# Performance work log

Measured on AMD Instinct MI355X. Metric: run time of the kernel, lower is better.

Reference implementation:

```python
import jax, jax.numpy as jnp
import numpy as np

B, T, N = 32, 64, 2048
HID, HEADS, DH, BOT, MAX_LAG = 256, 8, 32, 64, 7


def setup_inputs() -> dict:
    key = jax.random.key(0)
    ks = jax.random.split(key, 12)
    def nrm(k, shape, s=0.05):
        return jax.random.normal(k, shape, jnp.float32) * s
    # delay logits init as in the module: log(softmaxed exp decay)
    w = np.exp(-np.arange(MAX_LAG + 1) / 3.0)
    w = w / w.sum()
    delay_logits = jnp.asarray(np.log(w + 1e-8), jnp.float32)
    # row-normalized adjacency prior (done in __init__ of the module)
    adj_raw = jax.random.uniform(ks[0], (N, N), jnp.float32)
    adj_prior = adj_raw / (adj_raw.sum(-1, keepdims=True) + 1e-8)
    return {
        "x": jax.random.normal(ks[1], (B, T, N), jnp.float32),
        "features": jax.random.normal(ks[2], (B, N, HID), jnp.float32),
        "delay_logits": delay_logits,
        "w_dp": nrm(ks[3], (1, HID)), "b_dp": jnp.zeros((HID,), jnp.float32),
        "w_qkv_low": nrm(ks[4], (HID, 3 * BOT)), "b_qkv_low": jnp.zeros((3 * BOT,), jnp.float32),
        "w_qkv_high": nrm(ks[5], (3 * BOT, 3 * HID)), "b_qkv_high": jnp.zeros((3 * HID,), jnp.float32),
        "w_out_low": nrm(ks[6], (HID, BOT)), "b_out_low": jnp.zeros((BOT,), jnp.float32),
        "w_out_high": nrm(ks[7], (BOT, HID)), "b_out_high": jnp.zeros((HID,), jnp.float32),
        "adj_prior": adj_prior,
        "geo_weight": jnp.array([0.3], jnp.float32),
        "ln_gamma": jnp.ones((HID,), jnp.float32),
        "ln_beta": jnp.zeros((HID,), jnp.float32),
    }


def reference(x, features, delay_logits, w_dp, b_dp,
              w_qkv_low, b_qkv_low, w_qkv_high, b_qkv_high,
              w_out_low, b_out_low, w_out_high, b_out_high,
              adj_prior, geo_weight, ln_gamma, ln_beta):
    # --- delay-weighted signal (generation interval) ---
    dw = jax.nn.softmax(delay_logits)                      # [max_lag+1]
    taus = min(MAX_LAG + 1, T)                              # static
    x_lags = jnp.flip(x, axis=1)[:, :taus]                  # [B,taus,N], lag tau = x[:, -(tau+1)]
    delayed = jnp.einsum('t,btn->bn', dw[:taus], x_lags)    # [B,N]
    delay_feat = delayed[:, :, None] * w_dp[0] + b_dp       # Linear(1, hidden)
    combined = features + 0.1 * delay_feat                  # [B,N,HID]

    # --- low-rank QKV ---
    qkv = (combined @ w_qkv_low + b_qkv_low) @ w_qkv_high + b_qkv_high  # [B,N,3*HID]
    q, k, v = jnp.split(qkv, 3, axis=-1)
    def to_heads(t):
        return t.reshape(B, N, HEADS, DH).transpose(0, 2, 1, 3)  # [B,H,N,dh]
    q, k, v = to_heads(q), to_heads(k), to_heads(v)

    # --- linear attention (elu+1 feature map, O(N)) ---
    qf = jax.nn.elu(q) + 1.0
    kf = jax.nn.elu(k) + 1.0
    kv = jnp.einsum('bhnd,bhne->bhde', kf, v)               # [B,H,dh,dh]
    k_sum = kf.sum(axis=2) + 1e-8                           # [B,H,dh]
    num = jnp.einsum('bhnd,bhde->bhne', qf, kv)             # [B,H,N,dh]
    den = jnp.einsum('bhnd,bhd->bhn', qf, k_sum)[..., None] + 1e-8
    attended = num / den

    # --- geo-adjacency blend ---
    gb = jax.nn.sigmoid(geo_weight[0])
    v_geo = jnp.einsum('nm,bhmd->bhnd', adj_prior, v)       # dense graph mixing
    attended = (1.0 - gb) * attended + gb * v_geo

    attended = attended.transpose(0, 2, 1, 3).reshape(B, N, HID)
    # dropout is identity in eval mode
    out = (attended @ w_out_low + b_out_low) @ w_out_high + b_out_high

    # --- residual + LayerNorm ---
    y = out + features
    mu = y.mean(-1, keepdims=True)
    var = ((y - mu) ** 2).mean(-1, keepdims=True)
    return (y - mu) / jnp.sqrt(var + 1e-5) * ln_gamma + ln_beta
```

## Files before the change

kernel.cpp:

```cpp
#include <hip/hip_runtime.h>
#include <hip/hip_bf16.h>
#include <stdint.h>

typedef unsigned short u16;
typedef float f4v __attribute__((ext_vector_type(4)));
typedef short s8v __attribute__((ext_vector_type(8)));


__device__ __forceinline__ float bf2f(u16 u) {
  union { float f; uint32_t i; } x; x.i = ((uint32_t)u) << 16; return x.f;
}
__device__ __forceinline__ u16 f2bf(float f) {
  uint32_t u = __float_as_uint(f);
  u = (u + 0x7FFFu + ((u >> 16) & 1u)) >> 16;
  return (u16)u;
}
__device__ __forceinline__ uint32_t pk2(float a, float b) {
  return (uint32_t)f2bf(a) | ((uint32_t)f2bf(b) << 16);
}
__device__ __forceinline__ void gload16(const void* g, void* l) {
  __builtin_amdgcn_global_load_lds((const __attribute__((address_space(1))) void*)g,
                                   (__attribute__((address_space(3))) void*)l, 16, 0, 0);
}

__global__ __launch_bounds__(256) void prep_all_k(
    const float* __restrict__ x, const float* __restrict__ dlog,
    const float* __restrict__ w_dp, const float* __restrict__ b_dp,
    const float* __restrict__ wql, const float* __restrict__ bql,
    const float* __restrict__ wqh, const float* __restrict__ wol,
    const float* __restrict__ bqh,
    float* __restrict__ wl_d, float* __restrict__ bl_p, float* __restrict__ delayed,
    u16* __restrict__ wqlT, u16* __restrict__ wqhT, u16* __restrict__ wvlT,
    float* __restrict__ cvl) {
  const int bid = blockIdx.x, t = threadIdx.x;
  if (bid < 256) {
    float mx = dlog[0];
#pragma unroll
    for (int i = 1; i < 8; ++i) mx = fmaxf(mx, dlog[i]);
    float w8[8], ssum = 0.f;
#pragma unroll
    for (int i = 0; i < 8; ++i) { w8[i] = __expf(dlog[i] - mx); ssum += w8[i]; }
    float inv = 1.f / ssum;
    int r = bid * 256 + t;
    int b = r >> 11, n = r & 2047;
    const float* xb = x + (size_t)b * 64 * 2048;
    float acc = 0.f;
#pragma unroll
    for (int tau = 0; tau < 8; ++tau) acc += w8[tau] * inv * xb[(size_t)(63 - tau) * 2048 + n];
    delayed[r] = acc;
  } else if (bid < 512) {
    int n = bid - 256;
    wqlT[(size_t)n * 256 + t] = f2bf(n < 192 ? wql[(size_t)t * 192 + n] : 0.f);
  } else if (bid < 1280) {
    int n = bid - 512;
    if (t < 192) wqhT[(size_t)n * 192 + t] = f2bf(wqh[(size_t)t * 768 + n]);
  } else if (bid < 1408) {
    int d = bid - 1280;
    __shared__ float wolc[256];
    if (d < 64) wolc[t] = wol[(size_t)t * 64 + d];
    __syncthreads();
    if (t < 192) {
      float s = 0.f;
      if (d < 64) {
        const float* wr = wqh + (size_t)t * 768 + 512;
        for (int c = 0; c < 256; ++c) s = fmaf(wr[c], wolc[c], s);
      }
      wvlT[(size_t)d * 192 + t] = f2bf(s);
    }
    if (t == 0 && d < 64) {
      float s = 0.f;
      for (int c = 0; c < 256; ++c) s = fmaf(bqh[512 + c], wolc[c], s);
      cvl[d] = s;
    }
  } else {
    if (t < 192) {
      float s1 = 0.f, s2 = 0.f;
      for (int k = 0; k < 256; ++k) {
        float w = wql[k * 192 + t];
        s1 += w_dp[k] * w;
        s2 += b_dp[k] * w;
      }
      wl_d[t] = 0.1f * s1;
      bl_p[t] = bql[t] + 0.1f * s2;
    }
  }
}

struct MArgs {
  const u16* A;
  const float* Af32;
  const u16* Bt;
  const float* delayed; const float* wl_d; const float* bl_p;
  const float* bqh;
  const float* cvl;
  u16* low; u16* qf; u16* kf; u16* v; u16* vpt;
  u16* geopart;
};

enum { GLOW = 0, GQ = 1, GKV = 2, GGEO = 3, GVP = 4 };

template <int MODE>
__global__ __launch_bounds__(256) void mgemm_k(MArgs ma) {
  constexpr int KLOOP = (MODE == GLOW) ? 256 : (MODE == GGEO) ? 512 : 192;
  constexpr int LDA = (MODE == GLOW) ? 256 : (MODE == GGEO) ? 2048 : 192;
  constexpr int LDB = (MODE == GLOW) ? 256 : (MODE == GGEO) ? 2048 : 192;
  constexpr bool SWAPPED = (MODE == GLOW || MODE == GQ || MODE == GGEO);

  constexpr int SHN = (MODE == GKV) ? (128 * 136) : (128 * 128);
  __shared__ __align__(16) u16 SH[SHN];
  u16* Al = SH;
  u16* Bl = SH + 128 * 64;

  const int t = threadIdx.x;
  const int l = t & 63, w = t >> 6;
  const int wm = w >> 1, wn = w & 1;

  int ct, rt, bz = 0;
  if constexpr (MODE == GGEO) {
    int lin = blockIdx.x + 16 * blockIdx.y + 256 * blockIdx.z;
    int xcd = lin & 7, idx = lin >> 3;
    ct = idx & 15;
    int pid = xcd * 8 + (idx >> 4);
    rt = pid & 15;
    bz = pid >> 4;
  } else {
    constexpr int NCT = (MODE == GLOW || MODE == GQ) ? 2 : (MODE == GKV) ? 4 : 1;
    int lin = blockIdx.x + NCT * blockIdx.y;
    int xcd = lin & 7, idx = lin >> 3;
    ct = idx % NCT; rt = xcd * 64 + idx / NCT;
  }
  const int kbase = (MODE == GGEO) ? bz * 512 : 0;

  f4v acc[4][4] = {};

  for (int k0 = 0; k0 < KLOOP; k0 += 64) {
    __syncthreads();
#pragma unroll
    for (int s = 0; s < 4; ++s) {
      int c = s * 256 + t;
      int r = c >> 3, cc = c & 7;
      int g = ((cc & 3) ^ ((r >> 1) & 3)) | ((cc & 4) ^ ((r & 1) << 2));
      int row = rt * 128 + r;
      int kg = kbase + k0 + g * 8;
      if constexpr (MODE == GLOW || MODE == GGEO) {
        const float* src = ma.Af32 + (size_t)row * LDA + kg;
        float4 x0 = *(const float4*)src;
        float4 x1 = *(const float4*)(src + 4);
        uint4 qq = {pk2(x0.x, x0.y), pk2(x0.z, x0.w), pk2(x1.x, x1.y), pk2(x1.z, x1.w)};
        *(uint4*)&Al[c * 8] = qq;
      } else {
        gload16(ma.A + (size_t)row * LDA + kg, (char*)Al + (s * 4 + w) * 1024);
      }
      gload16(ma.Bt + (size_t)(ct * 128 + r) * LDB + kg,
              (char*)Bl + (s * 4 + w) * 1024);
    }
    __syncthreads();

#pragma unroll
    for (int kk = 0; kk < 64; kk += 32) {
      s8v fa[4], fb[4];
#pragma unroll
      for (int mr = 0; mr < 4; ++mr) {
        int ra = wm * 64 + mr * 16 + (l & 15);
        int ch = ((l >> 4) ^ ((ra >> 1) & 3)) | ((kk >> 3) ^ ((ra & 1) << 2));
        fa[mr] = *(const s8v*)(Al + ra * 64 + ch * 8);
      }
#pragma unroll
      for (int nr = 0; nr < 4; ++nr) {
        int rb = wn * 64 + nr * 16 + (l & 15);
        int cb = ((l >> 4) ^ ((rb >> 1) & 3)) | ((kk >> 3) ^ ((rb & 1) << 2));
        fb[nr] = *(const s8v*)(Bl + rb * 64 + cb * 8);
      }
      if constexpr (SWAPPED) {
#pragma unroll
        for (int mr = 0; mr < 4; ++mr)
#pragma unroll
          for (int nr = 0; nr < 4; ++nr)
            acc[mr][nr] = __builtin_amdgcn_mfma_f32_16x16x32_bf16(fb[nr], fa[mr], acc[mr][nr], 0, 0, 0);
      } else {
#pragma unroll
        for (int mr = 0; mr < 4; ++mr)
#pragma unroll
          for (int nr = 0; nr < 4; ++nr)
            acc[mr][nr] = __builtin_amdgcn_mfma_f32_16x16x32_bf16(fa[mr], fb[nr], acc[mr][nr], 0, 0, 0);
      }
    }
  }

  const int r0 = rt * 128 + wm * 64, c0 = ct * 128 + wn * 64;

  if constexpr (MODE == GVP) {
    const int lr = (l >> 4) * 4, lc = l & 15;
#pragma unroll
    for (int mr = 0; mr < 4; ++mr)
#pragma unroll
      for (int nr = 0; nr < 4; ++nr) {
        if (wn == 0) {
          int d = nr * 16 + lc;
          float cadd = ma.cvl[d];
          int n0 = (r0 + mr * 16 + lr) & 2047;
          int b = rt >> 4;
          ushort4 st = {f2bf(acc[mr][nr][0] + cadd), f2bf(acc[mr][nr][1] + cadd),
                        f2bf(acc[mr][nr][2] + cadd), f2bf(acc[mr][nr][3] + cadd)};
          *(ushort4*)(ma.vpt + ((size_t)(b * 64 + d)) * 2048 + n0) = st;
        }
      }
  } else if constexpr (MODE == GKV) {
    const int lr = (l >> 4) * 4, lc = l & 15;
    const bool isK = (ct < 2);
    __syncthreads();
#pragma unroll
    for (int nr = 0; nr < 4; ++nr) {
      int chat_l = wn * 64 + nr * 16 + lc;
      float bias = ma.bqh[256 + ct * 128 + chat_l];
#pragma unroll
      for (int mr = 0; mr < 4; ++mr) {
        int n_l = wm * 64 + mr * 16 + lr;
        float v0 = acc[mr][nr][0] + bias;
        float v1 = acc[mr][nr][1] + bias;
        float v2 = acc[mr][nr][2] + bias;
        float v3 = acc[mr][nr][3] + bias;
        if (isK) {
          v0 = (v0 > 0.f) ? (v0 + 1.f) : __expf(v0);
          v1 = (v1 > 0.f) ? (v1 + 1.f) : __expf(v1);
          v2 = (v2 > 0.f) ? (v2 + 1.f) : __expf(v2);
          v3 = (v3 > 0.f) ? (v3 + 1.f) : __expf(v3);
        }
        ushort4 st = {f2bf(v0), f2bf(v1), f2bf(v2), f2bf(v3)};
        *(ushort4*)&SH[chat_l * 136 + n_l] = st;
      }
    }
    __syncthreads();
    const int b = rt >> 4, nbase = (rt & 15) * 128;
#pragma unroll
    for (int s = 0; s < 8; ++s) {
      int idx = s * 256 + t;
      int chat_l = idx >> 4, nch = (idx & 15) * 8;
      uint4 q = *(const uint4*)&SH[chat_l * 136 + nch];
      int chat_g = ct * 128 + chat_l;
      u16* dst = isK ? (ma.kf + ((size_t)(b * 256 + chat_g)) * 2048)
                     : (ma.v + ((size_t)(b * 256 + chat_g - 256)) * 2048);
      *(uint4*)(dst + nbase + nch) = q;
    }
  } else {
    const int rowl = l & 15, colq = (l >> 4) * 4;
#pragma unroll
    for (int mr = 0; mr < 4; ++mr) {
      int row = r0 + mr * 16 + rowl;
#pragma unroll
      for (int nr = 0; nr < 4; ++nr) {
        int col0 = c0 + nr * 16 + colq;
        if constexpr (MODE == GLOW) {
          if (col0 < 192) {
            float dl = ma.delayed[row];
            float4 wd = *(const float4*)(ma.wl_d + col0);
            float4 bp = *(const float4*)(ma.bl_p + col0);
            ushort4 st = {f2bf(acc[mr][nr][0] + dl * wd.x + bp.x),
                          f2bf(acc[mr][nr][1] + dl * wd.y + bp.y),
                          f2bf(acc[mr][nr][2] + dl * wd.z + bp.z),
                          f2bf(acc[mr][nr][3] + dl * wd.w + bp.w)};
            *(ushort4*)(ma.low + (size_t)row * 192 + col0) = st;
          }
        } else if constexpr (MODE == GQ) {
          float4 bias = *(const float4*)(ma.bqh + col0);
          float v0 = acc[mr][nr][0] + bias.x;
          float v1 = acc[mr][nr][1] + bias.y;
          float v2 = acc[mr][nr][2] + bias.z;
          float v3 = acc[mr][nr][3] + bias.w;
          v0 = (v0 > 0.f) ? (v0 + 1.f) : __expf(v0);
          v1 = (v1 > 0.f) ? (v1 + 1.f) : __expf(v1);
          v2 = (v2 > 0.f) ? (v2 + 1.f) : __expf(v2);
          v3 = (v3 > 0.f) ? (v3 + 1.f) : __expf(v3);
          ushort4 st = {f2bf(v0), f2bf(v1), f2bf(v2), f2bf(v3)};
          *(ushort4*)(ma.qf + (size_t)row * 256 + col0) = st;
        } else {
          u16* dst = ma.geopart + (size_t)bz * 4194304;
          ushort4 st = {f2bf(acc[mr][nr][0]), f2bf(acc[mr][nr][1]),
                        f2bf(acc[mr][nr][2]), f2bf(acc[mr][nr][3])};
          *(ushort4*)(dst + (size_t)row * 2048 + col0) = st;
        }
      }
    }
  }
}

__global__ __launch_bounds__(256) void kvred_k(const u16* __restrict__ kfT,
                                               const u16* __restrict__ vT,
                                               float* __restrict__ kvpart,
                                               float* __restrict__ kspart) {
  const int z = blockIdx.x, h = blockIdx.y, b = blockIdx.z;
  const int t = threadIdx.x, l = t & 63, w = t >> 6;
  const size_t base = ((size_t)(b * 256 + h * 32)) * 2048 + z * 512 + w * 128;
  const u16* ka = kfT + base;
  const u16* vb = vT + base;
  f4v acc[2][2] = {};
  float ks[2] = {0.f, 0.f};
#pragma unroll
  for (int s = 0; s < 4; ++s) {
    int koff = s * 32 + (l >> 4) * 8;
    s8v fa[2], fb[2];
#pragma unroll
    for (int mr = 0; mr < 2; ++mr)
      fa[mr] = *(const s8v*)(ka + (size_t)(mr * 16 + (l & 15)) * 2048 + koff);
#pragma unroll
    for (int nr = 0; nr < 2; ++nr)
      fb[nr] = *(const s8v*)(vb + (size_t)(nr * 16 + (l & 15)) * 2048 + koff);
#pragma unroll
    for (int mr = 0; mr < 2; ++mr) {
      float sacc = 0.f;
#pragma unroll
      for (int j = 0; j < 8; ++j) sacc += bf2f((u16)fa[mr][j]);
      ks[mr] += sacc;
    }
#pragma unroll
    for (int mr = 0; mr < 2; ++mr)
#pragma unroll
      for (int nr = 0; nr < 2; ++nr)
        acc[mr][nr] = __builtin_amdgcn_mfma_f32_16x16x32_bf16(fa[mr], fb[nr], acc[mr][nr], 0, 0, 0);
  }
  ks[0] += __shfl_xor(ks[0], 16); ks[0] += __shfl_xor(ks[0], 32);
  ks[1] += __shfl_xor(ks[1], 16); ks[1] += __shfl_xor(ks[1], 32);

  __shared__ float kvs[4][32][32];
  __shared__ float kss[4][32];
#pragma unroll
  for (int mr = 0; mr < 2; ++mr)
#pragma unroll
    for (int nr = 0; nr < 2; ++nr)
#pragma unroll
      for (int i = 0; i < 4; ++i)
        kvs[w][mr * 16 + (l >> 4) * 4 + i][nr * 16 + (l & 15)] = acc[mr][nr][i];
  if (l < 16) { kss[w][l] = ks[0]; kss[w][16 + l] = ks[1]; }
  __syncthreads();
  float* kvp = kvpart + ((size_t)(z * 256 + b * 8 + h)) * 1024;
#pragma unroll
  for (int q = 0; q < 4; ++q) {
    int idx = q * 256 + t;
    kvp[idx] = kvs[0][idx >> 5][idx & 31] + kvs[1][idx >> 5][idx & 31] +
               kvs[2][idx >> 5][idx & 31] + kvs[3][idx >> 5][idx & 31];
  }
  if (t < 32)
    kspart[((size_t)(z * 256 + b * 8 + h)) * 32 + t] =
        kss[0][t] + kss[1][t] + kss[2][t] + kss[3][t];
}

__global__ __launch_bounds__(256) void gfin_k(const u16* __restrict__ qf,
                                              const float* __restrict__ rden,
                                              const u16* __restrict__ geopart,
                                              const u16* __restrict__ B2t,
                                              const float* __restrict__ cvec,
                                              const float* __restrict__ feats,
                                              const float* __restrict__ gamma,
                                              const float* __restrict__ beta,
                                              float* __restrict__ y) {
  __shared__ __align__(16) u16 Al[64 * 64];
  __shared__ __align__(16) u16 Bl[256 * 64];
  __shared__ float LN1[4][64], LN2[4][64];

  const int t = threadIdx.x;
  const int l = t & 63, w = t >> 6;
  const int rt = blockIdx.x;
  const int b = rt >> 5;

  f4v acc[4][4] = {};

  for (int k0 = 0; k0 < 320; k0 += 64) {
    __syncthreads();
#pragma unroll
    for (int s = 0; s < 2; ++s) {
      int c = s * 256 + t;
      int r = c >> 3, cc = c & 7;
      int g = ((cc & 3) ^ ((r >> 1) & 3)) | ((cc & 4) ^ ((r & 1) << 2));
      int row = rt * 64 + r;
      int kg = k0 + g * 8;
      if (k0 < 256) {
        float sc = rden[(size_t)row * 8 + (kg >> 5)];
        s8v qv = *(const s8v*)(qf + (size_t)row * 256 + kg);
        uint4 qq = {pk2(bf2f((u16)qv[0]) * sc, bf2f((u16)qv[1]) * sc),
                    pk2(bf2f((u16)qv[2]) * sc, bf2f((u16)qv[3]) * sc),
                    pk2(bf2f((u16)qv[4]) * sc, bf2f((u16)qv[5]) * sc),
                    pk2(bf2f((u16)qv[6]) * sc, bf2f((u16)qv[7]) * sc)};
        *(uint4*)&Al[c * 8] = qq;
      } else {
        int n = row & 2047;
        const u16* gp = geopart + (size_t)n * 2048 + b * 64 + (kg - 256);
        s8v p0 = *(const s8v*)(gp);
        s8v p1 = *(const s8v*)(gp + 4194304);
        s8v p2 = *(const s8v*)(gp + 8388608);
        s8v p3 = *(const s8v*)(gp + 12582912);
        float vv[8];
#pragma unroll
        for (int j = 0; j < 8; ++j)
          vv[j] = bf2f((u16)p0[j]) + bf2f((u16)p1[j]) + bf2f((u16)p2[j]) + bf2f((u16)p3[j]);
        uint4 qq = {pk2(vv[0], vv[1]), pk2(vv[2], vv[3]), pk2(vv[4], vv[5]), pk2(vv[6], vv[7])};
        *(uint4*)&Al[c * 8] = qq;
      }
    }
#pragma unroll
    for (int s = 0; s < 8; ++s) {
      int c = s * 256 + t;
      int r = c >> 3, cc = c & 7;
      int g = ((cc & 3) ^ ((r >> 1) & 3)) | ((cc & 4) ^ ((r & 1) << 2));
      gload16(B2t + ((size_t)b * 256 + r) * 320 + k0 + g * 8,
              (char*)Bl + (s * 4 + w) * 1024);
    }
    __syncthreads();

#pragma unroll
    for (int kk = 0; kk < 64; kk += 32) {
      s8v fa[4], fb[4];
#pragma unroll
      for (int mr = 0; mr < 4; ++mr) {
        int ra = mr * 16 + (l & 15);
        int ch = ((l >> 4) ^ ((ra >> 1) & 3)) | ((kk >> 3) ^ ((ra & 1) << 2));
        fa[mr] = *(const s8v*)(Al + ra * 64 + ch * 8);
      }
#pragma unroll
      for (int nr = 0; nr < 4; ++nr) {
        int rb = w * 64 + nr * 16 + (l & 15);
        int cb = ((l >> 4) ^ ((rb >> 1) & 3)) | ((kk >> 3) ^ ((rb & 1) << 2));
        fb[nr] = *(const s8v*)(Bl + rb * 64 + cb * 8);
      }
#pragma unroll
      for (int mr = 0; mr < 4; ++mr)
#pragma unroll
        for (int nr = 0; nr < 4; ++nr)
          acc[mr][nr] = __builtin_amdgcn_mfma_f32_16x16x32_bf16(fb[nr], fa[mr], acc[mr][nr], 0, 0, 0);
    }
  }

  const int rowl = l & 15, colq = (l >> 4) * 4;
  float s1v[4] = {0.f, 0.f, 0.f, 0.f}, s2v[4] = {0.f, 0.f, 0.f, 0.f};
#pragma unroll
  for (int mr = 0; mr < 4; ++mr) {
    int row = rt * 64 + mr * 16 + rowl;
#pragma unroll
    for (int nr = 0; nr < 4; ++nr) {
      int col0 = w * 64 + nr * 16 + colq;
      float4 cv = *(const float4*)(cvec + col0);
      float4 ft = *(const float4*)(feats + (size_t)row * 256 + col0);
      f4v vv = acc[mr][nr];
      vv[0] += cv.x + ft.x; vv[1] += cv.y + ft.y;
      vv[2] += cv.z + ft.z; vv[3] += cv.w + ft.w;
      acc[mr][nr] = vv;
      s1v[mr] += vv[0] + vv[1] + vv[2] + vv[3];
      s2v[mr] += vv[0] * vv[0] + vv[1] * vv[1] + vv[2] * vv[2] + vv[3] * vv[3];
    }
  }
#pragma unroll
  for (int mr = 0; mr < 4; ++mr) {
    s1v[mr] += __shfl_xor(s1v[mr], 16); s2v[mr] += __shfl_xor(s2v[mr], 16);
    s1v[mr] += __shfl_xor(s1v[mr], 32); s2v[mr] += __shfl_xor(s2v[mr], 32);
  }
  if (l < 16) {
#pragma unroll
    for (int mr = 0; mr < 4; ++mr) {
      LN1[w][mr * 16 + l] = s1v[mr];
      LN2[w][mr * 16 + l] = s2v[mr];
    }
  }
  __syncthreads();
#pragma unroll
  for (int mr = 0; mr < 4; ++mr) {
    int rl = mr * 16 + rowl;
    int row = rt * 64 + rl;
    float s1 = LN1[0][rl] + LN1[1][rl] + LN1[2][rl] + LN1[3][rl];
    float s2 = LN2[0][rl] + LN2[1][rl] + LN2[2][rl] + LN2[3][rl];
    float mu = s1 * (1.f / 256.f);
    float var = s2 * (1.f / 256.f) - mu * mu;
    float rstd = rsqrtf(fmaxf(var, 0.f) + 1e-5f);
#pragma unroll
    for (int nr = 0; nr < 4; ++nr) {
      int col0 = w * 64 + nr * 16 + colq;
      float4 g4 = *(const float4*)(gamma + col0);
      float4 b4 = *(const float4*)(beta + col0);
      f4v vv = acc[mr][nr];
      float4 o;
      o.x = (vv[0] - mu) * rstd * g4.x + b4.x;
      o.y = (vv[1] - mu) * rstd * g4.y + b4.y;
      o.z = (vv[2] - mu) * rstd * g4.z + b4.z;
      o.w = (vv[3] - mu) * rstd * g4.w + b4.w;
      *(float4*)(y + (size_t)row * 256 + col0) = o;
    }
  }
}

__global__ __launch_bounds__(64) void mmat_k(const float* __restrict__ kvpart,
                                             const float* __restrict__ wol,
                                             const float* __restrict__ geow,
                                             float* __restrict__ Mm) {
  const int bh = blockIdx.x;
  const int h = bh & 7, b = bh >> 3;
  const int c = threadIdx.x;
  __shared__ float kvs[32][32];
  for (int i = c; i < 1024; i += 64) {
    float s = 0.f;
#pragma unroll
    for (int p = 0; p < 4; ++p) s += kvpart[(size_t)(p * 256 + bh) * 1024 + i];
    kvs[i >> 5][i & 31] = s;
  }
  __syncthreads();
  float one_m = 1.f - 1.f / (1.f + __expf(-geow[0]));
  float acc[32];
#pragma unroll
  for (int d = 0; d < 32; ++d) acc[d] = 0.f;
  for (int e = 0; e < 32; ++e) {
    float w = wol[(size_t)(h * 32 + e) * 64 + c];
#pragma unroll
    for (int d = 0; d < 32; ++d) acc[d] = fmaf(kvs[d][e], w, acc[d]);
  }
  float* mp = Mm + (size_t)b * 16384 + (size_t)h * 32 * 64 + c;
#pragma unroll
  for (int d = 0; d < 32; ++d) mp[d * 64] = one_m * acc[d];
}

__global__ __launch_bounds__(256) void bprep_k(const float* __restrict__ Mm,
                                               const float* __restrict__ woh,
                                               const float* __restrict__ bol,
                                               const float* __restrict__ boh,
                                               const float* __restrict__ geow,
                                               u16* __restrict__ B2t,
                                               float* __restrict__ cvec) {
  const int kt = blockIdx.x, b = blockIdx.y;
  const int c = threadIdx.x;
  __shared__ float Ms[64][64];
#pragma unroll
  for (int i = 0; i < 16; ++i) {
    int flat = c + i * 256;
    int kk = flat >> 6, e = flat & 63;
    Ms[kk][e] = Mm[(size_t)b * 16384 + (size_t)(kt * 64 + kk) * 64 + e];
  }
  __syncthreads();
  float wcol[64];
#pragma unroll
  for (int e = 0; e < 64; ++e) wcol[e] = woh[(size_t)e * 256 + c];
  u16* dst = B2t + ((size_t)b * 256 + c) * 320;
  for (int kk = 0; kk < 64; ++kk) {
    float s = 0.f;
#pragma unroll
    for (int e = 0; e < 64; ++e) s = fmaf(Ms[kk][e], wcol[e], s);
    dst[kt * 64 + kk] = f2bf(s);
  }
  if (kt == 0) {
    float gb = 1.f / (1.f + __expf(-geow[0]));
#pragma unroll
    for (int d = 0; d < 64; ++d) dst[256 + d] = f2bf(gb * wcol[d]);
    if (b == 0) {
      float s = boh[c];
#pragma unroll
      for (int d = 0; d < 64; ++d) s = fmaf(bol[d], wcol[d], s);
      cvec[c] = s;
    }
  }
}

__global__ __launch_bounds__(256) void rden_k(const u16* __restrict__ qf,
                                              const float* __restrict__ kspart,
                                              float* __restrict__ rden) {
  const int t = threadIdx.x;
  const int b = (blockIdx.x * 16) >> 11;
  __shared__ float ksumf[256];
  {
    int h = t >> 5, e = t & 31;
    float s = 0.f;
#pragma unroll
    for (int p = 0; p < 4; ++p) s += kspart[(size_t)(p * 256 + b * 8 + h) * 32 + e];
    ksumf[t] = s + 1e-8f;
  }
  __syncthreads();
  const int row = blockIdx.x * 16 + (t >> 4);
  const int c0 = (t & 15) * 16;
  s8v q0 = *(const s8v*)(qf + (size_t)row * 256 + c0);
  s8v q1 = *(const s8v*)(qf + (size_t)row * 256 + c0 + 8);
  float part = 0.f;
#pragma unroll
  for (int j = 0; j < 8; ++j) part = fmaf(bf2f((u16)q0[j]), ksumf[c0 + j], part);
#pragma unroll
  for (int j = 0; j < 8; ++j) part = fmaf(bf2f((u16)q1[j]), ksumf[c0 + 8 + j], part);
  float den = part + __shfl_xor(part, 1);
  if ((t & 1) == 0) rden[(size_t)row * 8 + (c0 >> 5)] = 1.f / (den + 1e-8f);
}

extern "C" void kernel_launch(void* const* d_in, const int* in_sizes, int n_in,
                              void* d_out, int out_size, void* d_ws, size_t ws_size,
                              hipStream_t stream) {
  const float* x     = (const float*)d_in[0];
  const float* feats = (const float*)d_in[1];
  const float* dlog  = (const float*)d_in[2];
  const float* w_dp  = (const float*)d_in[3];
  const float* b_dp  = (const float*)d_in[4];
  const float* wql   = (const float*)d_in[5];
  const float* bql   = (const float*)d_in[6];
  const float* wqh   = (const float*)d_in[7];
  const float* bqh   = (const float*)d_in[8];
  const float* wol   = (const float*)d_in[9];
  const float* bol   = (const float*)d_in[10];
  const float* woh   = (const float*)d_in[11];
  const float* boh   = (const float*)d_in[12];
  const float* adj   = (const float*)d_in[13];
  const float* geow  = (const float*)d_in[14];
  const float* gamma = (const float*)d_in[15];
  const float* beta  = (const float*)d_in[16];

  char* ws = (char*)d_ws;
  constexpr size_t OFF_WLD   = 1024;
  constexpr size_t OFF_BLP   = 2048;
  constexpr size_t OFF_CVEC  = 4096;
  constexpr size_t OFF_CVL   = 5120;
  constexpr size_t OFF_DEL   = 8192;
  constexpr size_t OFF_WQLT  = 270336;
  constexpr size_t OFF_WQHT  = 401408;
  constexpr size_t OFF_WVLT  = 696320;
  constexpr size_t OFF_KSP   = 745472;
  constexpr size_t OFF_RDEN  = 876544;
  constexpr size_t OFF_MM    = 2973696;
  constexpr size_t OFF_B2T   = 5070848;
  constexpr size_t OFF_KVP   = OFF_B2T;
  constexpr size_t OFF_LOW   = 10444800;
  constexpr size_t OFF_QF    = 35610624;
  constexpr size_t OFF_KF    = 69165056;
  constexpr size_t OFF_VPT   = OFF_KF;
  constexpr size_t OFF_V     = 102719488;
  constexpr size_t OFF_GPART = OFF_V;

  float* wl_d    = (float*)(ws + OFF_WLD);
  float* bl_p    = (float*)(ws + OFF_BLP);
  float* cvec    = (float*)(ws + OFF_CVEC);
  float* cvl     = (float*)(ws + OFF_CVL);
  float* delayed = (float*)(ws + OFF_DEL);
  float* kspart  = (float*)(ws + OFF_KSP);
  float* rden    = (float*)(ws + OFF_RDEN);
  float* Mm      = (float*)(ws + OFF_MM);
  float* kvpart  = (float*)(ws + OFF_KVP);
  u16* wqlT = (u16*)(ws + OFF_WQLT);
  u16* wqhT = (u16*)(ws + OFF_WQHT);
  u16* wvlT = (u16*)(ws + OFF_WVLT);
  u16* B2t  = (u16*)(ws + OFF_B2T);

  MArgs ma{};
  ma.delayed = delayed; ma.wl_d = wl_d; ma.bl_p = bl_p; ma.bqh = bqh; ma.cvl = cvl;
  ma.low = (u16*)(ws + OFF_LOW);
  ma.qf  = (u16*)(ws + OFF_QF);
  ma.kf  = (u16*)(ws + OFF_KF);
  ma.v   = (u16*)(ws + OFF_V);
  ma.vpt = (u16*)(ws + OFF_VPT);
  ma.geopart = (u16*)(ws + OFF_GPART);

  prep_all_k<<<1409, 256, 0, stream>>>(x, dlog, w_dp, b_dp, wql, bql, wqh, wol, bqh,
                                       wl_d, bl_p, delayed, wqlT, wqhT, wvlT, cvl);

  MArgs m0 = ma; m0.Af32 = feats; m0.Bt = wqlT;
  mgemm_k<GLOW><<<dim3(2, 512), 256, 0, stream>>>(m0);

  MArgs m1 = ma; m1.A = ma.low; m1.Bt = wqhT;
  mgemm_k<GQ><<<dim3(2, 512), 256, 0, stream>>>(m1);

  MArgs m1b = ma; m1b.A = ma.low; m1b.Bt = wqhT + (size_t)256 * 192;
  mgemm_k<GKV><<<dim3(4, 512), 256, 0, stream>>>(m1b);

  kvred_k<<<dim3(4, 8, 32), 256, 0, stream>>>(ma.kf, ma.v, kvpart, kspart);
  mmat_k<<<256, 64, 0, stream>>>(kvpart, wol, geow, Mm);
  rden_k<<<4096, 256, 0, stream>>>(ma.qf, kspart, rden);
  bprep_k<<<dim3(4, 32), 256, 0, stream>>>(Mm, woh, bol, boh, geow, B2t, cvec);

  MArgs m2 = ma; m2.A = ma.low; m2.Bt = wvlT;
  mgemm_k<GVP><<<dim3(1, 512), 256, 0, stream>>>(m2);

  MArgs m3 = ma; m3.Af32 = adj; m3.Bt = ma.vpt;
  mgemm_k<GGEO><<<dim3(16, 16, 4), 256, 0, stream>>>(m3);

  gfin_k<<<1024, 256, 0, stream>>>(ma.qf, rden, ma.geopart, B2t, cvec,
                                   feats, gamma, beta, (float*)d_out);
  (void)in_sizes; (void)n_in; (void)out_size; (void)ws_size;
}
```

Before: 266.7 us.

## Drop LDS staging in gfin_k; each wave owns 16 full rows, direct global fragment loads

The final GEMM+LayerNorm kernel no longer stages A and B tiles through shared memory with swizzles and barriers. Each wave now computes 16 complete output rows across all 256 columns, loading its A fragments and B fragments straight from global memory into registers. The LayerNorm reduction then needs only in-wave shuffles, so the LDS buffers and cross-wave sums go away. The cost is that B2t is reread from global/L2 by every wave with no LDS sharing, and each lane holds 16 accumulators.

```diff
diff --git a/kernel.cpp b/kernel.cpp
--- a/kernel.cpp
+++ b/kernel.cpp
@@ -353,135 +353,84 @@
                                               const float* __restrict__ gamma,
                                               const float* __restrict__ beta,
                                               float* __restrict__ y) {
-  __shared__ __align__(16) u16 Al[64 * 64];
-  __shared__ __align__(16) u16 Bl[256 * 64];
-  __shared__ float LN1[4][64], LN2[4][64];
-
   const int t = threadIdx.x;
   const int l = t & 63, w = t >> 6;
   const int rt = blockIdx.x;
   const int b = rt >> 5;
-
-  f4v acc[4][4] = {};
-
-  for (int k0 = 0; k0 < 320; k0 += 64) {
-    __syncthreads();
-#pragma unroll
-    for (int s = 0; s < 2; ++s) {
-      int c = s * 256 + t;
-      int r = c >> 3, cc = c & 7;
-      int g = ((cc & 3) ^ ((r >> 1) & 3)) | ((cc & 4) ^ ((r & 1) << 2));
-      int row = rt * 64 + r;
-      int kg = k0 + g * 8;
-      if (k0 < 256) {
-        float sc = rden[(size_t)row * 8 + (kg >> 5)];
-        s8v qv = *(const s8v*)(qf + (size_t)row * 256 + kg);
-        uint4 qq = {pk2(bf2f((u16)qv[0]) * sc, bf2f((u16)qv[1]) * sc),
-                    pk2(bf2f((u16)qv[2]) * sc, bf2f((u16)qv[3]) * sc),
-                    pk2(bf2f((u16)qv[4]) * sc, bf2f((u16)qv[5]) * sc),
-                    pk2(bf2f((u16)qv[6]) * sc, bf2f((u16)qv[7]) * sc)};
-        *(uint4*)&Al[c * 8] = qq;
-      } else {
-        int n = row & 2047;
-        const u16* gp = geopart + (size_t)n * 2048 + b * 64 + (kg - 256);
-        s8v p0 = *(const s8v*)(gp);
-        s8v p1 = *(const s8v*)(gp + 4194304);
-        s8v p2 = *(const s8v*)(gp + 8388608);
-        s8v p3 = *(const s8v*)(gp + 12582912);
-        float vv[8];
-#pragma unroll
-        for (int j = 0; j < 8; ++j)
-          vv[j] = bf2f((u16)p0[j]) + bf2f((u16)p1[j]) + bf2f((u16)p2[j]) + bf2f((u16)p3[j]);
-        uint4 qq = {pk2(vv[0], vv[1]), pk2(vv[2], vv[3]), pk2(vv[4], vv[5]), pk2(vv[6], vv[7])};
-        *(uint4*)&Al[c * 8] = qq;
-      }
-    }
-#pragma unroll
-    for (int s = 0; s < 8; ++s) {
-      int c = s * 256 + t;
-      int r = c >> 3, cc = c & 7;
-      int g = ((cc & 3) ^ ((r >> 1) & 3)) | ((cc & 4) ^ ((r & 1) << 2));
-      gload16(B2t + ((size_t)b * 256 + r) * 320 + k0 + g * 8,
-              (char*)Bl + (s * 4 + w) * 1024);
-    }
-    __syncthreads();
-
-#pragma unroll
-    for (int kk = 0; kk < 64; kk += 32) {
-      s8v fa[4], fb[4];
-#pragma unroll
-      for (int mr = 0; mr < 4; ++mr) {
-        int ra = mr * 16 + (l & 15);
-        int ch = ((l >> 4) ^ ((ra >> 1) & 3)) | ((kk >> 3) ^ ((ra & 1) << 2));
-        fa[mr] = *(const s8v*)(Al + ra * 64 + ch * 8);
-      }
-#pragma unroll
-      for (int nr = 0; nr < 4; ++nr) {
-        int rb = w * 64 + nr * 16 + (l & 15);
-        int cb = ((l >> 4) ^ ((rb >> 1) & 3)) | ((kk >> 3) ^ ((rb & 1) << 2));
-        fb[nr] = *(const s8v*)(Bl + rb * 64 + cb * 8);
-      }
-#pragma unroll
-      for (int mr = 0; mr < 4; ++mr)
-#pragma unroll
-        for (int nr = 0; nr < 4; ++nr)
-          acc[mr][nr] = __builtin_amdgcn_mfma_f32_16x16x32_bf16(fb[nr], fa[mr], acc[mr][nr], 0, 0, 0);
-    }
-  }
-
-  const int rowl = l & 15, colq = (l >> 4) * 4;
-  float s1v[4] = {0.f, 0.f, 0.f, 0.f}, s2v[4] = {0.f, 0.f, 0.f, 0.f};
-#pragma unroll
-  for (int mr = 0; mr < 4; ++mr) {
-    int row = rt * 64 + mr * 16 + rowl;
-#pragma unroll
-    for (int nr = 0; nr < 4; ++nr) {
-      int col0 = w * 64 + nr * 16 + colq;
-      float4 cv = *(const float4*)(cvec + col0);
-      float4 ft = *(const float4*)(feats + (size_t)row * 256 + col0);
-      f4v vv = acc[mr][nr];
-      vv[0] += cv.x + ft.x; vv[1] += cv.y + ft.y;
-      vv[2] += cv.z + ft.z; vv[3] += cv.w + ft.w;
-      acc[mr][nr] = vv;
-      s1v[mr] += vv[0] + vv[1] + vv[2] + vv[3];
-      s2v[mr] += vv[0] * vv[0] + vv[1] * vv[1] + vv[2] * vv[2] + vv[3] * vv[3];
-    }
-  }
-#pragma unroll
-  for (int mr = 0; mr < 4; ++mr) {
-    s1v[mr] += __shfl_xor(s1v[mr], 16); s2v[mr] += __shfl_xor(s2v[mr], 16);
-    s1v[mr] += __shfl_xor(s1v[mr], 32); s2v[mr] += __shfl_xor(s2v[mr], 32);
-  }
-  if (l < 16) {
-#pragma unroll
-    for (int mr = 0; mr < 4; ++mr) {
-      LN1[w][mr * 16 + l] = s1v[mr];
-      LN2[w][mr * 16 + l] = s2v[mr];
-    }
-  }
-  __syncthreads();
-#pragma unroll
-  for (int mr = 0; mr < 4; ++mr) {
-    int rl = mr * 16 + rowl;
-    int row = rt * 64 + rl;
-    float s1 = LN1[0][rl] + LN1[1][rl] + LN1[2][rl] + LN1[3][rl];
-    float s2 = LN2[0][rl] + LN2[1][rl] + LN2[2][rl] + LN2[3][rl];
-    float mu = s1 * (1.f / 256.f);
-    float var = s2 * (1.f / 256.f) - mu * mu;
-    float rstd = rsqrtf(fmaxf(var, 0.f) + 1e-5f);
-#pragma unroll
-    for (int nr = 0; nr < 4; ++nr) {
-      int col0 = w * 64 + nr * 16 + colq;
-      float4 g4 = *(const float4*)(gamma + col0);
-      float4 b4 = *(const float4*)(beta + col0);
-      f4v vv = acc[mr][nr];
-      float4 o;
-      o.x = (vv[0] - mu) * rstd * g4.x + b4.x;
-      o.y = (vv[1] - mu) * rstd * g4.y + b4.y;
-      o.z = (vv[2] - mu) * rstd * g4.z + b4.z;
-      o.w = (vv[3] - mu) * rstd * g4.w + b4.w;
-      *(float4*)(y + (size_t)row * 256 + col0) = o;
-    }
+  const int lrow = l & 15, lko = (l >> 4) * 8;
+  const int row = rt * 64 + w * 16 + lrow;
+
+  const u16* Bb = B2t + (size_t)b * 256 * 320;
+  const u16* qr = qf + (size_t)row * 256;
+
+  f4v acc[16] = {};
+  union { uint4 q; s8v v; } fau;
+
+#pragma unroll
+  for (int k0 = 0; k0 < 320; k0 += 32) {
+    const int kg = k0 + lko;
+    if (k0 < 256) {
+      float sc = rden[(size_t)row * 8 + (k0 >> 5)];
+      s8v qv = *(const s8v*)(qr + kg);
+      fau.q.x = pk2(bf2f((u16)qv[0]) * sc, bf2f((u16)qv[1]) * sc);
+      fau.q.y = pk2(bf2f((u16)qv[2]) * sc, bf2f((u16)qv[3]) * sc);
+      fau.q.z = pk2(bf2f((u16)qv[4]) * sc, bf2f((u16)qv[5]) * sc);
+      fau.q.w = pk2(bf2f((u16)qv[6]) * sc, bf2f((u16)qv[7]) * sc);
+    } else {
+      int n = row & 2047;
+      const u16* gp = geopart + (size_t)n * 2048 + b * 64 + (kg - 256);
+      s8v p0 = *(const s8v*)(gp);
+      s8v p1 = *(const s8v*)(gp + 4194304);
+      s8v p2 = *(const s8v*)(gp + 8388608);
+      s8v p3 = *(const s8v*)(gp + 12582912);
+      float vv[8];
+#pragma unroll
+      for (int j = 0; j < 8; ++j)
+        vv[j] = bf2f((u16)p0[j]) + bf2f((u16)p1[j]) + bf2f((u16)p2[j]) + bf2f((u16)p3[j]);
+      fau.q.x = pk2(vv[0], vv[1]);
+      fau.q.y = pk2(vv[2], vv[3]);
+      fau.q.z = pk2(vv[4], vv[5]);
+      fau.q.w = pk2(vv[6], vv[7]);
+    }
+    s8v fa = fau.v;
+#pragma unroll
+    for (int nr = 0; nr < 16; ++nr) {
+      s8v fb = *(const s8v*)(Bb + (size_t)(nr * 16 + lrow) * 320 + kg);
+      acc[nr] = __builtin_amdgcn_mfma_f32_16x16x32_bf16(fb, fa, acc[nr], 0, 0, 0);
+    }
+  }
+
+  const int colq = (l >> 4) * 4;
+  float s1 = 0.f, s2 = 0.f;
+#pragma unroll
+  for (int nr = 0; nr < 16; ++nr) {
+    int col0 = nr * 16 + colq;
+    float4 cv = *(const float4*)(cvec + col0);
+    float4 ft = *(const float4*)(feats + (size_t)row * 256 + col0);
+    f4v vv = acc[nr];
+    vv[0] += cv.x + ft.x; vv[1] += cv.y + ft.y;
+    vv[2] += cv.z + ft.z; vv[3] += cv.w + ft.w;
+    acc[nr] = vv;
+    s1 += vv[0] + vv[1] + vv[2] + vv[3];
+    s2 += vv[0] * vv[0] + vv[1] * vv[1] + vv[2] * vv[2] + vv[3] * vv[3];
+  }
+  s1 += __shfl_xor(s1, 16); s1 += __shfl_xor(s1, 32);
+  s2 += __shfl_xor(s2, 16); s2 += __shfl_xor(s2, 32);
+  float mu = s1 * (1.f / 256.f);
+  float var = s2 * (1.f / 256.f) - mu * mu;
+  float rstd = rsqrtf(fmaxf(var, 0.f) + 1e-5f);
+#pragma unroll
+  for (int nr = 0; nr < 16; ++nr) {
+    int col0 = nr * 16 + colq;
+    float4 g4 = *(const float4*)(gamma + col0);
+    float4 b4 = *(const float4*)(beta + col0);
+    f4v vv = acc[nr];
+    float4 o;
+    o.x = (vv[0] - mu) * rstd * g4.x + b4.x;
+    o.y = (vv[1] - mu) * rstd * g4.y + b4.y;
+    o.z = (vv[2] - mu) * rstd * g4.z + b4.z;
+    o.w = (vv[3] - mu) * rstd * g4.w + b4.w;
+    *(float4*)(y + (size_t)row * 256 + col0) = o;
   }
 }
 
```

New measurement: 315.8 us. 1.18x slower.
